# Optimization experiments

Measured on AMD Instinct MI355X. Metric: run time of the kernel, lower is better.

The kernel has to match this reference:

```python
import jax, jax.numpy as jnp
import numpy as np

LN_EPS = 1e-5

def setup_inputs() -> dict:
    key = jax.random.key(0)
    ks = jax.random.split(key, 6)
    N, CD, CC, CF = 500000, 64, 96, 128
    return {
        "x_detial": jax.random.normal(ks[0], (N, CD), dtype=jnp.float32),
        "x_context": jax.random.normal(ks[1], (N, CC), dtype=jnp.float32),
        "W_detial": jax.random.normal(ks[2], (CD, CF), dtype=jnp.float32) * 0.05,
        "W_context": jax.random.normal(ks[3], (CC, CF), dtype=jnp.float32) * 0.05,
        "W_gate1": jax.random.normal(ks[4], (CD + CC, CF // 2), dtype=jnp.float32) * 0.05,
        "ln_gamma": jnp.ones((CF // 2,), dtype=jnp.float32),
        "ln_beta": jnp.zeros((CF // 2,), dtype=jnp.float32),
        "W_gate2": jax.random.normal(ks[5], (CF // 2, 1), dtype=jnp.float32) * 0.05,
    }

def _layer_norm(x, gamma, beta):
    mu = jnp.mean(x, axis=-1, keepdims=True)
    var = jnp.mean(jnp.square(x - mu), axis=-1, keepdims=True)
    return (x - mu) * jax.lax.rsqrt(var + LN_EPS) * gamma + beta

def reference(x_detial, x_context, W_detial, W_context, W_gate1, ln_gamma, ln_beta, W_gate2):
    # gate path: 1x1 subm conv == per-point linear on [N, C] features
    concat = jnp.concatenate([x_detial, x_context], axis=1)        # [N, CD+CC]
    h = jnp.matmul(concat, W_gate1)                                 # [N, CF//2]
    h = jax.nn.relu(_layer_norm(h, ln_gamma, ln_beta))
    gate = jax.nn.sigmoid(jnp.matmul(h, W_gate2))                   # [N, 1]
    detail_aligned = jnp.matmul(x_detial, W_detial)                 # [N, CF]
    context_aligned = jnp.matmul(x_context, W_context)              # [N, CF]
    return (1.0 - gate) * context_aligned + gate * detail_aligned   # [N, CF]
```

## Files before the change

kernel.cpp:

```cpp
#include <hip/hip_runtime.h>
#include <hip/hip_bf16.h>
#include <math.h>


namespace {

typedef __attribute__((ext_vector_type(8))) short short8;
typedef __attribute__((ext_vector_type(4))) float f32x4;

constexpr int CD = 64, CC = 96, CH = 64, CF = 128;
constexpr int NFG1 = 20;
constexpr int NFCB = 40;
constexpr int NFRAG = NFG1 + NFCB;
constexpr int WCHUNKS = NFRAG * 512 * 2 / 16;

__device__ inline short bf16_of(float f) {
  __hip_bfloat16 h = __float2bfloat16(f);
  return *reinterpret_cast<short*>(&h);
}

__global__ void convert_weights(const float* __restrict__ Wd,
                                const float* __restrict__ Wc,
                                const float* __restrict__ Wg1,
                                short* __restrict__ ws) {
  const int t = blockIdx.x * 256 + threadIdx.x;
  if (t >= 64 * NFRAG) return;
  const int frag = t >> 6, l = t & 63;
  const int cidx = l & 15, kb = l >> 4;
  float v[8];
  if (frag < NFG1) {
    const int ks = frag >> 2, nt = frag & 3;
    const int n = nt * 16 + cidx, k0 = ks * 32 + kb * 8;
    #pragma unroll
    for (int j = 0; j < 8; ++j) v[j] = Wg1[(k0 + j) * CH + n];
  } else {
    const int f2 = frag - NFG1;
    const int ks = f2 >> 3, nt = f2 & 7;
    const int n = nt * 16 + cidx, k0 = ks * 32 + kb * 8;
    #pragma unroll
    for (int j = 0; j < 8; ++j) {
      const int k = k0 + j;
      v[j] = (k < CD) ? Wd[k * CF + n] : Wc[(k - CD) * CF + n];
    }
  }
  short8 o;
  #pragma unroll
  for (int j = 0; j < 8; ++j) o[j] = bf16_of(v[j]);
  *reinterpret_cast<short8*>(ws + frag * 512 + l * 8) = o;
}

__global__ __launch_bounds__(512, 4)
void gate_fusion_mfma(const float* __restrict__ xd,
                      const float* __restrict__ xc,
                      const float* __restrict__ gma,
                      const float* __restrict__ bta,
                      const float* __restrict__ Wg2,
                      const short* __restrict__ wf,
                      float* __restrict__ out, int N) {
  __shared__ short wlds[NFRAG * 512];

  const int tid  = threadIdx.x;
  const int lane = tid & 63;
  const int wv   = tid >> 6;
  const int r0   = blockIdx.x * 256 + wv * 32;
  const int cidx = lane & 15;
  const int kb   = lane >> 4;
  const bool active = (r0 < N);

  f32x4 buf[2][5][2];
  if (active) {
    #pragma unroll
    for (int mt = 0; mt < 2; ++mt) {
      const size_t row = (size_t)(r0 + mt * 16 + cidx);
      const float* rd = xd + row * CD + kb * 8;
      const float* rc = xc + row * CC + kb * 8;
      #pragma unroll
      for (int ks = 0; ks < 5; ++ks) {
        const float* p = (ks < 2) ? (rd + ks * 32) : (rc + (ks - 2) * 32);
        buf[mt][ks][0] = *reinterpret_cast<const f32x4*>(p);
        buf[mt][ks][1] = *reinterpret_cast<const f32x4*>(p + 4);
      }
    }
  }

  for (int c = tid; c < WCHUNKS; c += 512) {
    short8 v = *reinterpret_cast<const short8*>(wf + (size_t)c * 8);
    *reinterpret_cast<short8*>(&wlds[c * 8]) = v;
  }
  __syncthreads();
  if (!active) return;

  float gmv[4], btv[4], w2v[4];
  #pragma unroll
  for (int nt = 0; nt < 4; ++nt) {
    const int c = nt * 16 + cidx;
    gmv[nt] = gma[c]; btv[nt] = bta[c]; w2v[nt] = Wg2[c];
  }

  short8 xf[2][5];
  #pragma unroll
  for (int mt = 0; mt < 2; ++mt)
    #pragma unroll
    for (int ks = 0; ks < 5; ++ks) {
      short8 f;
      #pragma unroll
      for (int j = 0; j < 4; ++j) {
        f[j]     = bf16_of(buf[mt][ks][0][j]);
        f[4 + j] = bf16_of(buf[mt][ks][1][j]);
      }
      xf[mt][ks] = f;
    }

  const f32x4 vzero = {0.f, 0.f, 0.f, 0.f};
  f32x4 acc1[2][4];
  #pragma unroll
  for (int mt = 0; mt < 2; ++mt)
    #pragma unroll
    for (int nt = 0; nt < 4; ++nt) acc1[mt][nt] = vzero;

  #pragma unroll
  for (int ks = 0; ks < 5; ++ks) {
    short8 bg[4];
    #pragma unroll
    for (int nt = 0; nt < 4; ++nt)
      bg[nt] = *reinterpret_cast<const short8*>(&wlds[(ks * 4 + nt) * 512 + lane * 8]);
    #pragma unroll
    for (int mt = 0; mt < 2; ++mt)
      #pragma unroll
      for (int nt = 0; nt < 4; ++nt)
        acc1[mt][nt] = __builtin_amdgcn_mfma_f32_16x16x32_bf16(
            xf[mt][ks], bg[nt], acc1[mt][nt], 0, 0, 0);
  }

  float gate[2][4];
  #pragma unroll
  for (int mt = 0; mt < 2; ++mt) {
    float s[4], q[4];
    #pragma unroll
    for (int r = 0; r < 4; ++r) {
      s[r] = 0.f; q[r] = 0.f;
      #pragma unroll
      for (int nt = 0; nt < 4; ++nt) {
        const float c = acc1[mt][nt][r];
        s[r] += c; q[r] += c * c;
      }
    }
    #pragma unroll
    for (int m = 1; m < 16; m <<= 1)
      #pragma unroll
      for (int r = 0; r < 4; ++r) {
        s[r] += __shfl_xor(s[r], m, 64);
        q[r] += __shfl_xor(q[r], m, 64);
      }
    float p[4];
    #pragma unroll
    for (int r = 0; r < 4; ++r) {
      const float mu  = s[r] * (1.f / CH);
      const float var = q[r] * (1.f / CH) - mu * mu;
      const float rsd = rsqrtf(var + 1e-5f);
      float pp = 0.f;
      #pragma unroll
      for (int nt = 0; nt < 4; ++nt) {
        const float h = fmaxf((acc1[mt][nt][r] - mu) * rsd * gmv[nt] + btv[nt], 0.f);
        pp += h * w2v[nt];
      }
      p[r] = pp;
    }
    #pragma unroll
    for (int m = 1; m < 16; m <<= 1)
      #pragma unroll
      for (int r = 0; r < 4; ++r) p[r] += __shfl_xor(p[r], m, 64);
    #pragma unroll
    for (int r = 0; r < 4; ++r) gate[mt][r] = 1.f / (1.f + expf(-p[r]));
  }

  #pragma unroll
  for (int q = 0; q < 4; ++q) {
    f32x4 aD[2][2], aC[2][2];
    #pragma unroll
    for (int mt = 0; mt < 2; ++mt)
      #pragma unroll
      for (int nt = 0; nt < 2; ++nt) { aD[mt][nt] = vzero; aC[mt][nt] = vzero; }

    #pragma unroll
    for (int ks = 0; ks < 5; ++ks) {
      short8 bg[2];
      #pragma unroll
      for (int nt = 0; nt < 2; ++nt)
        bg[nt] = *reinterpret_cast<const short8*>(
            &wlds[(NFG1 + ks * 8 + q * 2 + nt) * 512 + lane * 8]);
      if (ks < 2) {
        #pragma unroll
        for (int mt = 0; mt < 2; ++mt)
          #pragma unroll
          for (int nt = 0; nt < 2; ++nt)
            aD[mt][nt] = __builtin_amdgcn_mfma_f32_16x16x32_bf16(
                xf[mt][ks], bg[nt], aD[mt][nt], 0, 0, 0);
      } else {
        #pragma unroll
        for (int mt = 0; mt < 2; ++mt)
          #pragma unroll
          for (int nt = 0; nt < 2; ++nt)
            aC[mt][nt] = __builtin_amdgcn_mfma_f32_16x16x32_bf16(
                xf[mt][ks], bg[nt], aC[mt][nt], 0, 0, 0);
      }
    }

    #pragma unroll
    for (int mt = 0; mt < 2; ++mt) {
      const size_t rowb = (size_t)r0 + mt * 16 + kb * 4;
      #pragma unroll
      for (int nt = 0; nt < 2; ++nt) {
        #pragma unroll
        for (int r = 0; r < 4; ++r) {
          const float g = gate[mt][r];
          const float o = fmaf(g, aD[mt][nt][r] - aC[mt][nt][r], aC[mt][nt][r]);
          out[(rowb + r) * CF + (q * 2 + nt) * 16 + cidx] = o;
        }
      }
    }
  }
}

}

extern "C" void kernel_launch(void* const* d_in, const int* in_sizes, int n_in,
                              void* d_out, int out_size, void* d_ws, size_t ws_size,
                              hipStream_t stream) {
  const float* xd  = (const float*)d_in[0];
  const float* xc  = (const float*)d_in[1];
  const float* Wd  = (const float*)d_in[2];
  const float* Wc  = (const float*)d_in[3];
  const float* Wg1 = (const float*)d_in[4];
  const float* gma = (const float*)d_in[5];
  const float* bta = (const float*)d_in[6];
  const float* Wg2 = (const float*)d_in[7];
  float* out = (float*)d_out;
  short* ws  = (short*)d_ws;

  const int N = in_sizes[0] / CD;

  convert_weights<<<dim3(15), dim3(256), 0, stream>>>(Wd, Wc, Wg1, ws);

  const int nblk = (N + 255) / 256;
  gate_fusion_mfma<<<dim3(nblk), dim3(512), 0, stream>>>(
      xd, xc, gma, bta, Wg2, ws, out, N);
}
```

Baseline: 139.4 us.

## Process multiple row tiles per wave with register prefetch of next tile

Each wave now handles four consecutive 32-row tiles instead of one. The LDS weight staging is amortized over four tiles, and the next tile's inputs are loaded into registers while the current tile is computed. This cuts the number of blocks and repeated weight copies and overlaps global loads with MFMA work. In exchange there are fewer blocks to spread across CUs, and rows beyond a multiple of 32 are dropped because nTiles = N/32 truncates; that is harmless only when N is divisible by 32, as it is here.

```diff
diff --git a/kernel.cpp b/kernel.cpp
--- a/kernel.cpp
+++ b/kernel.cpp
@@ -13,6 +13,7 @@
 constexpr int NFCB = 40;
 constexpr int NFRAG = NFG1 + NFCB;
 constexpr int WCHUNKS = NFRAG * 512 * 2 / 16;
+constexpr int TPW = 4;
 
 __device__ inline short bf16_of(float f) {
   __hip_bfloat16 h = __float2bfloat16(f);
@@ -56,22 +57,21 @@
                       const float* __restrict__ bta,
                       const float* __restrict__ Wg2,
                       const short* __restrict__ wf,
-                      float* __restrict__ out, int N) {
+                      float* __restrict__ out, int nTiles) {
   __shared__ short wlds[NFRAG * 512];
 
   const int tid  = threadIdx.x;
   const int lane = tid & 63;
   const int wv   = tid >> 6;
-  const int r0   = blockIdx.x * 256 + wv * 32;
+  const int tb   = (blockIdx.x * 8 + wv) * TPW;
   const int cidx = lane & 15;
   const int kb   = lane >> 4;
-  const bool active = (r0 < N);
 
   f32x4 buf[2][5][2];
-  if (active) {
+  if (tb < nTiles) {
     #pragma unroll
     for (int mt = 0; mt < 2; ++mt) {
-      const size_t row = (size_t)(r0 + mt * 16 + cidx);
+      const size_t row = (size_t)tb * 32 + mt * 16 + cidx;
       const float* rd = xd + row * CD + kb * 8;
       const float* rc = xc + row * CC + kb * 8;
       #pragma unroll
@@ -88,7 +88,7 @@
     *reinterpret_cast<short8*>(&wlds[c * 8]) = v;
   }
   __syncthreads();
-  if (!active) return;
+  if (tb >= nTiles) return;
 
   float gmv[4], btv[4], w2v[4];
   #pragma unroll
@@ -97,125 +97,147 @@
     gmv[nt] = gma[c]; btv[nt] = bta[c]; w2v[nt] = Wg2[c];
   }
 
-  short8 xf[2][5];
-  #pragma unroll
-  for (int mt = 0; mt < 2; ++mt)
+  const f32x4 vzero = {0.f, 0.f, 0.f, 0.f};
+
+  for (int i = 0; i < TPW; ++i) {
+    const int t = tb + i;
+    if (t >= nTiles) break;
+
+    short8 xf[2][5];
+    #pragma unroll
+    for (int mt = 0; mt < 2; ++mt)
+      #pragma unroll
+      for (int ks = 0; ks < 5; ++ks) {
+        short8 f;
+        #pragma unroll
+        for (int j = 0; j < 4; ++j) {
+          f[j]     = bf16_of(buf[mt][ks][0][j]);
+          f[4 + j] = bf16_of(buf[mt][ks][1][j]);
+        }
+        xf[mt][ks] = f;
+      }
+
+    const int tn = t + 1;
+    if (i + 1 < TPW && tn < nTiles) {
+      #pragma unroll
+      for (int mt = 0; mt < 2; ++mt) {
+        const size_t row = (size_t)tn * 32 + mt * 16 + cidx;
+        const float* rd = xd + row * CD + kb * 8;
+        const float* rc = xc + row * CC + kb * 8;
+        #pragma unroll
+        for (int ks = 0; ks < 5; ++ks) {
+          const float* p = (ks < 2) ? (rd + ks * 32) : (rc + (ks - 2) * 32);
+          buf[mt][ks][0] = *reinterpret_cast<const f32x4*>(p);
+          buf[mt][ks][1] = *reinterpret_cast<const f32x4*>(p + 4);
+        }
+      }
+    }
+
+    f32x4 acc1[2][4];
+    #pragma unroll
+    for (int mt = 0; mt < 2; ++mt)
+      #pragma unroll
+      for (int nt = 0; nt < 4; ++nt) acc1[mt][nt] = vzero;
+
     #pragma unroll
     for (int ks = 0; ks < 5; ++ks) {
-      short8 f;
-      #pragma unroll
-      for (int j = 0; j < 4; ++j) {
-        f[j]     = bf16_of(buf[mt][ks][0][j]);
-        f[4 + j] = bf16_of(buf[mt][ks][1][j]);
-      }
-      xf[mt][ks] = f;
-    }
-
-  const f32x4 vzero = {0.f, 0.f, 0.f, 0.f};
-  f32x4 acc1[2][4];
-  #pragma unroll
-  for (int mt = 0; mt < 2; ++mt)
-    #pragma unroll
-    for (int nt = 0; nt < 4; ++nt) acc1[mt][nt] = vzero;
-
-  #pragma unroll
-  for (int ks = 0; ks < 5; ++ks) {
-    short8 bg[4];
-    #pragma unroll
-    for (int nt = 0; nt < 4; ++nt)
-      bg[nt] = *reinterpret_cast<const short8*>(&wlds[(ks * 4 + nt) * 512 + lane * 8]);
-    #pragma unroll
-    for (int mt = 0; mt < 2; ++mt)
+      short8 bg[4];
       #pragma unroll
       for (int nt = 0; nt < 4; ++nt)
-        acc1[mt][nt] = __builtin_amdgcn_mfma_f32_16x16x32_bf16(
-            xf[mt][ks], bg[nt], acc1[mt][nt], 0, 0, 0);
-  }
-
-  float gate[2][4];
-  #pragma unroll
-  for (int mt = 0; mt < 2; ++mt) {
-    float s[4], q[4];
-    #pragma unroll
-    for (int r = 0; r < 4; ++r) {
-      s[r] = 0.f; q[r] = 0.f;
-      #pragma unroll
-      for (int nt = 0; nt < 4; ++nt) {
-        const float c = acc1[mt][nt][r];
-        s[r] += c; q[r] += c * c;
-      }
-    }
-    #pragma unroll
-    for (int m = 1; m < 16; m <<= 1)
+        bg[nt] = *reinterpret_cast<const short8*>(&wlds[(ks * 4 + nt) * 512 + lane * 8]);
+      #pragma unroll
+      for (int mt = 0; mt < 2; ++mt)
+        #pragma unroll
+        for (int nt = 0; nt < 4; ++nt)
+          acc1[mt][nt] = __builtin_amdgcn_mfma_f32_16x16x32_bf16(
+              xf[mt][ks], bg[nt], acc1[mt][nt], 0, 0, 0);
+    }
+
+    float gate[2][4];
+    #pragma unroll
+    for (int mt = 0; mt < 2; ++mt) {
+      float s[4], q[4];
       #pragma unroll
       for (int r = 0; r < 4; ++r) {
-        s[r] += __shfl_xor(s[r], m, 64);
-        q[r] += __shfl_xor(q[r], m, 64);
-      }
-    float p[4];
-    #pragma unroll
-    for (int r = 0; r < 4; ++r) {
-      const float mu  = s[r] * (1.f / CH);
-      const float var = q[r] * (1.f / CH) - mu * mu;
-      const float rsd = rsqrtf(var + 1e-5f);
-      float pp = 0.f;
-      #pragma unroll
-      for (int nt = 0; nt < 4; ++nt) {
-        const float h = fmaxf((acc1[mt][nt][r] - mu) * rsd * gmv[nt] + btv[nt], 0.f);
-        pp += h * w2v[nt];
-      }
-      p[r] = pp;
-    }
-    #pragma unroll
-    for (int m = 1; m < 16; m <<= 1)
-      #pragma unroll
-      for (int r = 0; r < 4; ++r) p[r] += __shfl_xor(p[r], m, 64);
-    #pragma unroll
-    for (int r = 0; r < 4; ++r) gate[mt][r] = 1.f / (1.f + expf(-p[r]));
-  }
-
-  #pragma unroll
-  for (int q = 0; q < 4; ++q) {
-    f32x4 aD[2][2], aC[2][2];
-    #pragma unroll
-    for (int mt = 0; mt < 2; ++mt)
-      #pragma unroll
-      for (int nt = 0; nt < 2; ++nt) { aD[mt][nt] = vzero; aC[mt][nt] = vzero; }
-
-    #pragma unroll
-    for (int ks = 0; ks < 5; ++ks) {
-      short8 bg[2];
-      #pragma unroll
-      for (int nt = 0; nt < 2; ++nt)
-        bg[nt] = *reinterpret_cast<const short8*>(
-            &wlds[(NFG1 + ks * 8 + q * 2 + nt) * 512 + lane * 8]);
-      if (ks < 2) {
-        #pragma unroll
-        for (int mt = 0; mt < 2; ++mt)
+        s[r] = 0.f; q[r] = 0.f;
+        #pragma unroll
+        for (int nt = 0; nt < 4; ++nt) {
+          const float c = acc1[mt][nt][r];
+          s[r] += c; q[r] += c * c;
+        }
+      }
+      #pragma unroll
+      for (int m = 1; m < 16; m <<= 1)
+        #pragma unroll
+        for (int r = 0; r < 4; ++r) {
+          s[r] += __shfl_xor(s[r], m, 64);
+          q[r] += __shfl_xor(q[r], m, 64);
+        }
+      float p[4];
+      #pragma unroll
+      for (int r = 0; r < 4; ++r) {
+        const float mu  = s[r] * (1.f / CH);
+        const float var = q[r] * (1.f / CH) - mu * mu;
+        const float rsd = rsqrtf(var + 1e-5f);
+        float pp = 0.f;
+        #pragma unroll
+        for (int nt = 0; nt < 4; ++nt) {
+          const float h = fmaxf((acc1[mt][nt][r] - mu) * rsd * gmv[nt] + btv[nt], 0.f);
+          pp += h * w2v[nt];
+        }
+        p[r] = pp;
+      }
+      #pragma unroll
+      for (int m = 1; m < 16; m <<= 1)
+        #pragma unroll
+        for (int r = 0; r < 4; ++r) p[r] += __shfl_xor(p[r], m, 64);
+      #pragma unroll
+      for (int r = 0; r < 4; ++r) gate[mt][r] = 1.f / (1.f + expf(-p[r]));
+    }
+
+    #pragma unroll
+    for (int q = 0; q < 4; ++q) {
+      f32x4 aD[2][2], aC[2][2];
+      #pragma unroll
+      for (int mt = 0; mt < 2; ++mt)
+        #pragma unroll
+        for (int nt = 0; nt < 2; ++nt) { aD[mt][nt] = vzero; aC[mt][nt] = vzero; }
+
+      #pragma unroll
+      for (int ks = 0; ks < 5; ++ks) {
+        short8 bg[2];
+        #pragma unroll
+        for (int nt = 0; nt < 2; ++nt)
+          bg[nt] = *reinterpret_cast<const short8*>(
+              &wlds[(NFG1 + ks * 8 + q * 2 + nt) * 512 + lane * 8]);
+        if (ks < 2) {
           #pragma unroll
-          for (int nt = 0; nt < 2; ++nt)
-            aD[mt][nt] = __builtin_amdgcn_mfma_f32_16x16x32_bf16(
-                xf[mt][ks], bg[nt], aD[mt][nt], 0, 0, 0);
-      } else {
-        #pragma unroll
-        for (int mt = 0; mt < 2; ++mt)
+          for (int mt = 0; mt < 2; ++mt)
+            #pragma unroll
+            for (int nt = 0; nt < 2; ++nt)
+              aD[mt][nt] = __builtin_amdgcn_mfma_f32_16x16x32_bf16(
+                  xf[mt][ks], bg[nt], aD[mt][nt], 0, 0, 0);
+        } else {
           #pragma unroll
-          for (int nt = 0; nt < 2; ++nt)
-            aC[mt][nt] = __builtin_amdgcn_mfma_f32_16x16x32_bf16(
-                xf[mt][ks], bg[nt], aC[mt][nt], 0, 0, 0);
-      }
-    }
-
-    #pragma unroll
-    for (int mt = 0; mt < 2; ++mt) {
-      const size_t rowb = (size_t)r0 + mt * 16 + kb * 4;
-      #pragma unroll
-      for (int nt = 0; nt < 2; ++nt) {
-        #pragma unroll
-        for (int r = 0; r < 4; ++r) {
-          const float g = gate[mt][r];
-          const float o = fmaf(g, aD[mt][nt][r] - aC[mt][nt][r], aC[mt][nt][r]);
-          out[(rowb + r) * CF + (q * 2 + nt) * 16 + cidx] = o;
+          for (int mt = 0; mt < 2; ++mt)
+            #pragma unroll
+            for (int nt = 0; nt < 2; ++nt)
+              aC[mt][nt] = __builtin_amdgcn_mfma_f32_16x16x32_bf16(
+                  xf[mt][ks], bg[nt], aC[mt][nt], 0, 0, 0);
+        }
+      }
+
+      #pragma unroll
+      for (int mt = 0; mt < 2; ++mt) {
+        const size_t rowb = (size_t)t * 32 + mt * 16 + kb * 4;
+        #pragma unroll
+        for (int nt = 0; nt < 2; ++nt) {
+          #pragma unroll
+          for (int r = 0; r < 4; ++r) {
+            const float g = gate[mt][r];
+            const float o = fmaf(g, aD[mt][nt][r] - aC[mt][nt][r], aC[mt][nt][r]);
+            out[(rowb + r) * CF + (q * 2 + nt) * 16 + cidx] = o;
+          }
         }
       }
     }
@@ -239,10 +261,12 @@
   short* ws  = (short*)d_ws;
 
   const int N = in_sizes[0] / CD;
+  const int nTiles = N / 32;
 
   convert_weights<<<dim3(15), dim3(256), 0, stream>>>(Wd, Wc, Wg1, ws);
 
-  const int nblk = (N + 255) / 256;
+  const int tilesPerBlock = 8 * TPW;
+  const int nblk = (nTiles + tilesPerBlock - 1) / tilesPerBlock;
   gate_fusion_mfma<<<dim3(nblk), dim3(512), 0, stream>>>(
-      xd, xc, gma, bta, Wg2, ws, out, N);
-}
+      xd, xc, gma, bta, Wg2, ws, out, nTiles);
+}
```

Measured after the change: 305.3 us. +119.0%, slower.
